# Kernel tuning notes

Measured on AMD Instinct MI355X. Metric: run time of the kernel, lower is better.

Reference implementation:

```python
import jax, jax.numpy as jnp
import numpy as np

B, L, HID, H, D = 1, 2048, 3072, 24, 128
MLP = 4 * HID
LH, LW = 32, 56      # latent mask grid -> LH*LW image tokens at the END of the sequence
LIP = 16             # IP-adapter image tokens
IP_SCALE = 0.6


def setup_inputs() -> dict:
    key = jax.random.key(0)
    k = jax.random.split(key, 10)
    # Flux rotary pe layout [1,1,L,D//2,2,2]: pe[...,0]=[cos,-sin], pe[...,1]=[sin,cos]
    pos = jnp.arange(L, dtype=jnp.float32)
    freqs = 1.0 / (10000.0 ** (jnp.arange(0, D, 2, dtype=jnp.float32) / D))
    ang = pos[:, None] * freqs[None, :]            # [L, D//2]
    cos, sin = jnp.cos(ang), jnp.sin(ang)
    pe = jnp.stack([jnp.stack([cos, -sin], -1), jnp.stack([sin, cos], -1)], -2)[None, None]
    return {
        "x": jax.random.normal(k[0], (B, L, HID), jnp.float32),
        "vec": jax.random.normal(k[1], (B, HID), jnp.float32),
        "pe": pe,
        "img_mask": jax.random.uniform(k[2], (B, LH, LW), jnp.float32),
        "image_emb": jax.random.normal(k[3], (B, LIP, HID), jnp.float32),
        "mod_w": jax.random.normal(k[4], (3 * HID, HID), jnp.float32) * 0.02,
        "mod_b": jnp.zeros((3 * HID,), jnp.float32),
        "lin1_w": jax.random.normal(k[5], (3 * HID + MLP, HID), jnp.float32) * 0.02,
        "lin1_b": jnp.zeros((3 * HID + MLP,), jnp.float32),
        "q_scale": jnp.ones((D,), jnp.float32),
        "k_scale": jnp.ones((D,), jnp.float32),
        "lin2_w": jax.random.normal(k[6], (HID, HID + MLP), jnp.float32) * 0.02,
        "lin2_b": jnp.zeros((HID,), jnp.float32),
        "ipk_w": jax.random.normal(k[7], (HID, HID), jnp.float32) * 0.02,
        "ipv_w": jax.random.normal(k[8], (HID, HID), jnp.float32) * 0.02,
    }


def _rms(x, scale, eps):
    # RMSNorm over last dim (QKNorm / norm_added_k)
    return x * jax.lax.rsqrt(jnp.mean(x * x, -1, keepdims=True) + eps) * scale


def _apply_rope(x, pe):
    # x: [B,H,L,D]; pe: [1,1,L,D//2,2,2]
    xr = x.reshape(x.shape[:-1] + (D // 2, 1, 2))
    out = pe[..., 0] * xr[..., 0] + pe[..., 1] * xr[..., 1]  # [B,H,L,D//2,2]
    return out.reshape(x.shape)


def _sdpa(q, k, v):
    # q:[B,H,Lq,D] k,v:[B,H,Lk,D] -> [B,Lq,H*D]
    s = jnp.einsum('bhqd,bhkd->bhqk', q, k) / jnp.sqrt(jnp.float32(D))
    o = jnp.einsum('bhqk,bhkd->bhqd', jax.nn.softmax(s, -1), v)
    return o.transpose(0, 2, 1, 3).reshape(q.shape[0], q.shape[2], H * D)


def reference(x, vec, pe, img_mask, image_emb, mod_w, mod_b, lin1_w, lin1_b,
              q_scale, k_scale, lin2_w, lin2_b, ipk_w, ipv_w):
    # modulation: SiLU(vec) -> Linear -> (shift, scale, gate), each [B,1,HID]
    mod = jax.nn.silu(vec) @ mod_w.T + mod_b
    shift, scale, gate = [m[:, None, :] for m in jnp.split(mod, 3, -1)]
    # pre_norm: LayerNorm, no affine, eps 1e-6 (biased variance, matches torch)
    ln = (x - jnp.mean(x, -1, keepdims=True)) * jax.lax.rsqrt(jnp.var(x, -1, keepdims=True) + 1e-6)
    x_mod = (1.0 + scale) * ln + shift
    # fused qkv + mlp projection
    h = x_mod @ lin1_w.T + lin1_b
    qkv, mlp = h[..., :3 * HID], h[..., 3 * HID:]
    q, k, v = qkv.reshape(B, L, 3, H, D).transpose(2, 0, 3, 1, 4)  # each [B,H,L,D]
    q = _rms(q, q_scale, 1e-6)
    k = _rms(k, k_scale, 1e-6)
    # rp_attention: RoPE then SDPA
    attn = _sdpa(_apply_rope(q, pe), _apply_rope(k, pe), v)       # [B,L,HID]
    # IP-adapter cross-attention: pre-rope q attends to projected image_emb
    ip_k = _rms((image_emb @ ipk_w.T).reshape(B, LIP, H, D).transpose(0, 2, 1, 3), 1.0, 1e-5)
    ip_v = (image_emb @ ipv_w.T).reshape(B, LIP, H, D).transpose(0, 2, 1, 3)
    ip_h = IP_SCALE * _sdpa(q, ip_k, ip_v)                        # [B,L,HID]
    # spatial mask applied to last LH*LW tokens, zeros elsewhere
    full_mask = jnp.concatenate(
        [jnp.zeros((B, L - LH * LW), ip_h.dtype), img_mask.reshape(B, LH * LW)], 1)
    attn = attn + ip_h * full_mask[..., None]
    out = jnp.concatenate([attn, jax.nn.gelu(mlp, approximate=True)], -1) @ lin2_w.T + lin2_b
    return x + gate * out
```

## Files before the change

kernel.cpp:

```cpp
#include <hip/hip_runtime.h>

#define HID 3072
#define LSEQ 2048
#define NH 24
#define HD 128
#define N1 21504
#define K2 15360

typedef unsigned short ushort_t;
typedef __attribute__((ext_vector_type(8))) short bf16x8;
typedef __attribute__((ext_vector_type(4))) float f32x4;

__device__ __forceinline__ unsigned short f2bf(float f) {
    union { float f; unsigned int u; } v; v.f = f;
    unsigned int u = v.u;
    u += 0x7fffu + ((u >> 16) & 1u);
    return (unsigned short)(u >> 16);
}
__device__ __forceinline__ float bf2f(unsigned short s) {
    union { unsigned int u; float f; } v; v.u = ((unsigned int)s) << 16;
    return v.f;
}
__device__ __forceinline__ float gelu_tanh(float x) {
    float u = 0.7978845608028654f * (x + 0.044715f * x * x * x);
    float t = 2.0f / (1.0f + __expf(-2.0f * u)) - 1.0f;
    return 0.5f * x * (1.0f + t);
}
__device__ __forceinline__ void gload_lds16(const ushort_t* g, ushort_t* l) {
    __builtin_amdgcn_global_load_lds((const __attribute__((address_space(1))) void*)g,
                                     (__attribute__((address_space(3))) void*)l, 16, 0, 0);
}

__global__ __launch_bounds__(256) void k_cvt(const float* __restrict__ src,
    ushort_t* __restrict__ dst, int n)
{
    int stride = gridDim.x * 256 * 8;
    for (int i = (blockIdx.x * 256 + threadIdx.x) * 8; i < n; i += stride) {
        float4 a = *reinterpret_cast<const float4*>(src + i);
        float4 b = *reinterpret_cast<const float4*>(src + i + 4);
        uint4 pk;
        pk.x = (unsigned)f2bf(a.x) | ((unsigned)f2bf(a.y) << 16);
        pk.y = (unsigned)f2bf(a.z) | ((unsigned)f2bf(a.w) << 16);
        pk.z = (unsigned)f2bf(b.x) | ((unsigned)f2bf(b.y) << 16);
        pk.w = (unsigned)f2bf(b.z) | ((unsigned)f2bf(b.w) << 16);
        *reinterpret_cast<uint4*>(dst + i) = pk;
    }
}

__global__ __launch_bounds__(256) void k_mod(const float* __restrict__ vec,
    const float* __restrict__ mw, const float* __restrict__ mb, float* __restrict__ mod) {
    __shared__ __align__(16) float sv[HID];
    int tid = threadIdx.x;
    for (int i = tid; i < HID; i += 256) {
        float v = vec[i];
        sv[i] = v / (1.0f + __expf(-v));
    }
    __syncthreads();
    int wave = tid >> 6, lane = tid & 63;
    int n = blockIdx.x * 4 + wave;
    const float* w = mw + (size_t)n * HID;
    float acc = 0.0f;
    for (int k = lane * 4; k < HID; k += 256) {
        float4 wv = *reinterpret_cast<const float4*>(w + k);
        float4 s  = *reinterpret_cast<const float4*>(sv + k);
        acc += wv.x * s.x + wv.y * s.y + wv.z * s.z + wv.w * s.w;
    }
    #pragma unroll
    for (int off = 1; off < 64; off <<= 1) acc += __shfl_xor(acc, off);
    if (lane == 0) mod[n] = acc + mb[n];
}

__global__ __launch_bounds__(256) void k_lnmod(const float* __restrict__ x,
    const float* __restrict__ mod, ushort_t* __restrict__ xmod) {
    int row = blockIdx.x, tid = threadIdx.x;
    const float4* xr = reinterpret_cast<const float4*>(x + (size_t)row * HID);
    float4 v[3];
    float s = 0.f, sq = 0.f;
    #pragma unroll
    for (int i = 0; i < 3; ++i) {
        v[i] = xr[tid + i * 256];
        s  += v[i].x + v[i].y + v[i].z + v[i].w;
        sq += v[i].x * v[i].x + v[i].y * v[i].y + v[i].z * v[i].z + v[i].w * v[i].w;
    }
    #pragma unroll
    for (int off = 1; off < 64; off <<= 1) { s += __shfl_xor(s, off); sq += __shfl_xor(sq, off); }
    __shared__ float rs[4], rq[4];
    int wave = tid >> 6, lane = tid & 63;
    if (lane == 0) { rs[wave] = s; rq[wave] = sq; }
    __syncthreads();
    s  = rs[0] + rs[1] + rs[2] + rs[3];
    sq = rq[0] + rq[1] + rq[2] + rq[3];
    float mean = s * (1.0f / HID);
    float var = sq * (1.0f / HID) - mean * mean;
    float rstd = rsqrtf(var + 1e-6f);
    ushort_t* orow = xmod + (size_t)row * HID;
    #pragma unroll
    for (int i = 0; i < 3; ++i) {
        int c = (tid + i * 256) * 4;
        float4 sc = *reinterpret_cast<const float4*>(mod + HID + c);
        float4 sh = *reinterpret_cast<const float4*>(mod + c);
        float o0 = (1.f + sc.x) * ((v[i].x - mean) * rstd) + sh.x;
        float o1 = (1.f + sc.y) * ((v[i].y - mean) * rstd) + sh.y;
        float o2 = (1.f + sc.z) * ((v[i].z - mean) * rstd) + sh.z;
        float o3 = (1.f + sc.w) * ((v[i].w - mean) * rstd) + sh.w;
        *reinterpret_cast<ushort4*>(orow + c) = make_ushort4(f2bf(o0), f2bf(o1), f2bf(o2), f2bf(o3));
    }
}

#define MFMA_CLUSTER(PH, AF)                                                          \
    do {                                                                              \
        __builtin_amdgcn_s_setprio(1);                                                \
        _Pragma("unroll") for (int i_ = 0; i_ < 2; ++i_)                              \
        _Pragma("unroll") for (int nj_ = 0; nj_ < 4; ++nj_)                           \
        _Pragma("unroll") for (int kh_ = 0; kh_ < 2; ++kh_)                           \
            acc[2 * (PH) + i_][nj_] = __builtin_amdgcn_mfma_f32_16x16x32_bf16(        \
                AF[i_][kh_], bfrag[nj_][kh_], acc[2 * (PH) + i_][nj_], 0, 0, 0);      \
        __builtin_amdgcn_s_setprio(0);                                                \
    } while (0)

template<int EPI>
__global__ __launch_bounds__(512) void k_gemm8(
    const ushort_t* __restrict__ A, const ushort_t* __restrict__ W,
    const float* __restrict__ bias, int Ks, int klen,
    ushort_t* __restrict__ out_qkv, ushort_t* __restrict__ out_concat,
    float* __restrict__ part)
{
    extern __shared__ __align__(16) char smem_raw[];
    ushort_t* smem = (ushort_t*)smem_raw;
    int tid = threadIdx.x;
    int wid = tid >> 6, l = tid & 63;
    int wm = wid >> 2, wn = wid & 3;
    int lr = l & 15, lg = l >> 4;

    int NTILE = (EPI == 1) ? 84 : 12;
    int flat = blockIdx.y * NTILE + blockIdx.x;
    int nf = (flat & 7) * NTILE + (flat >> 3);
    int mt = nf & 7, nt = nf >> 3;
    int m0 = mt * 256, n0 = nt * 256;
    int koff = blockIdx.z * klen;
    int NT = klen >> 6;

    int lrow = l >> 3;
    int lc   = (l & 7) ^ lrow;
    int arow_st = wm * 128 + wn * 32 + lrow;
    int bhalf = wn >> 1, ridx = wm * 2 + (wn & 1);
    int brow_st = bhalf * 128 + ridx * 32 + lrow;
    const ushort_t* aSrc = A + (size_t)(m0 + arow_st) * Ks + koff + lc * 8;
    const ushort_t* bSrc = W + (size_t)(n0 + brow_st) * Ks + koff + lc * 8;
    int aDst = (wm * 128 + wn * 32) * 64;
    int bDst = (bhalf * 128 + ridx * 32) * 64;

    auto stageA = [&](int t, int buf, int c) {
        gload_lds16(aSrc + (size_t)c * 8 * Ks + (size_t)t * 64,
                    smem + buf * 16384 + aDst + c * 512);
    };
    auto stageB = [&](int t, int c) {
        gload_lds16(bSrc + (size_t)c * 8 * Ks + (size_t)t * 64,
                    smem + 49152 + (t & 1) * 16384 + bDst + c * 512);
    };
    auto readA = [&](int buf, int row, int ccc) {
        return *reinterpret_cast<const bf16x8*>(smem + buf * 16384 + row * 64 + ((ccc ^ (row & 7)) << 3));
    };
    auto readB = [&](int p, int row, int ccc) {
        return *reinterpret_cast<const bf16x8*>(smem + 49152 + p * 16384 + row * 64 + ((ccc ^ (row & 7)) << 3));
    };

    f32x4 acc[8][4] = {};

    #pragma unroll
    for (int c = 0; c < 4; ++c) stageA(0, 0, c);
    #pragma unroll
    for (int c = 0; c < 4; ++c) stageB(0, c);
    #pragma unroll
    for (int c = 0; c < 4; ++c) stageA(1, 1, c);
    #pragma unroll
    for (int c = 0; c < 4; ++c) stageB(1, c);
    asm volatile("s_waitcnt vmcnt(8)" ::: "memory");
    __builtin_amdgcn_s_barrier();

    int pA = 0;
    int pA2 = 2;
    for (int t = 0; t < NT; ++t) {
        int pB = t & 1;
        bf16x8 bfrag[4][2], af0[2][2], af1[2][2], af2[2][2], af3[2][2];
        #pragma unroll
        for (int nj = 0; nj < 4; ++nj)
            #pragma unroll
            for (int kh = 0; kh < 2; ++kh)
                bfrag[nj][kh] = readB(pB, wn * 64 + nj * 16 + lr, kh * 4 + lg);
        #pragma unroll
        for (int i = 0; i < 2; ++i)
            #pragma unroll
            for (int kh = 0; kh < 2; ++kh)
                af0[i][kh] = readA(pA, wm * 128 + i * 16 + lr, kh * 4 + lg);
        if (t + 2 < NT) {
            stageA(t + 2, pA2, 0); stageA(t + 2, pA2, 1);
            stageA(t + 2, pA2, 2); stageA(t + 2, pA2, 3);
        }
        #pragma unroll
        for (int i = 0; i < 2; ++i)
            #pragma unroll
            for (int kh = 0; kh < 2; ++kh)
                af1[i][kh] = readA(pA, wm * 128 + (2 + i) * 16 + lr, kh * 4 + lg);
        MFMA_CLUSTER(0, af0);
        #pragma unroll
        for (int i = 0; i < 2; ++i)
            #pragma unroll
            for (int kh = 0; kh < 2; ++kh)
                af2[i][kh] = readA(pA, wm * 128 + (4 + i) * 16 + lr, kh * 4 + lg);
        MFMA_CLUSTER(1, af1);
        __builtin_amdgcn_s_barrier();
        if (t + 2 < NT) {
            stageB(t + 2, 0); stageB(t + 2, 1);
            stageB(t + 2, 2); stageB(t + 2, 3);
        }
        #pragma unroll
        for (int i = 0; i < 2; ++i)
            #pragma unroll
            for (int kh = 0; kh < 2; ++kh)
                af3[i][kh] = readA(pA, wm * 128 + (6 + i) * 16 + lr, kh * 4 + lg);
        MFMA_CLUSTER(2, af2);
        MFMA_CLUSTER(3, af3);
        if (t + 2 < NT)      asm volatile("s_waitcnt vmcnt(8)" ::: "memory");
        else if (t + 1 < NT) asm volatile("s_waitcnt vmcnt(0)" ::: "memory");
        __builtin_amdgcn_s_barrier();
        pA  = (pA  + 1 == 3) ? 0 : pA  + 1;
        pA2 = (pA2 + 1 == 3) ? 0 : pA2 + 1;
    }

    #pragma unroll
    for (int nj = 0; nj < 4; ++nj) {
        int col = n0 + wn * 64 + nj * 16 + lr;
        float b = (EPI == 1) ? bias[col] : 0.f;
        #pragma unroll
        for (int mi = 0; mi < 8; ++mi) {
            int rbase = m0 + wm * 128 + mi * 16 + lg * 4;
            #pragma unroll
            for (int r = 0; r < 4; ++r) {
                int mrow = rbase + r;
                float val = acc[mi][nj][r] + b;
                if (EPI == 1) {
                    if (col < 3 * HID) {
                        out_qkv[(size_t)mrow * (3 * HID) + col] = f2bf(val);
                    } else {
                        out_concat[(size_t)mrow * K2 + HID + (col - 3 * HID)] = f2bf(gelu_tanh(val));
                    }
                } else {
                    part[(size_t)blockIdx.z * LSEQ * HID + (size_t)mrow * HID + col] = val;
                }
            }
        }
    }
}

__global__ __launch_bounds__(256) void k_red(const float* __restrict__ part,
    const float* __restrict__ bias, const float* __restrict__ xres,
    const float* __restrict__ mod, float* __restrict__ dout)
{
    size_t base = ((size_t)blockIdx.x * 256 + threadIdx.x) * 4;
    int col = (int)(base % HID);
    float4 s = *reinterpret_cast<const float4*>(part + base);
    #pragma unroll
    for (int z = 1; z < 8; ++z) {
        float4 p = *reinterpret_cast<const float4*>(part + (size_t)z * LSEQ * HID + base);
        s.x += p.x; s.y += p.y; s.z += p.z; s.w += p.w;
    }
    float4 bb = *reinterpret_cast<const float4*>(bias + col);
    float4 gg = *reinterpret_cast<const float4*>(mod + 2 * HID + col);
    float4 xx = *reinterpret_cast<const float4*>(xres + base);
    float4 o;
    o.x = xx.x + gg.x * (s.x + bb.x);
    o.y = xx.y + gg.y * (s.y + bb.y);
    o.z = xx.z + gg.z * (s.z + bb.z);
    o.w = xx.w + gg.w * (s.w + bb.w);
    *reinterpret_cast<float4*>(dout + base) = o;
}

__global__ __launch_bounds__(256) void k_qkv(const ushort_t* __restrict__ qkv,
    const float* __restrict__ pe, const float* __restrict__ q_scale, const float* __restrict__ k_scale,
    ushort_t* __restrict__ q_rope, ushort_t* __restrict__ k_rope,
    ushort_t* __restrict__ q_rms, ushort_t* __restrict__ v_t)
{
    __shared__ ushort_t vtile[64][132];
    int h = blockIdx.y, l0 = blockIdx.x * 64;
    int wave = threadIdx.x >> 6, lane = threadIdx.x & 63;
    int d0 = lane * 2;
    float qs0 = q_scale[d0], qs1 = q_scale[d0 + 1];
    float ks0 = k_scale[d0], ks1 = k_scale[d0 + 1];
    for (int it = 0; it < 16; ++it) {
        int ll = it * 4 + wave;
        int l = l0 + ll;
        const ushort_t* base = qkv + (size_t)l * (3 * HID) + h * HD + d0;
        unsigned qw = *reinterpret_cast<const unsigned*>(base);
        unsigned kw = *reinterpret_cast<const unsigned*>(base + HID);
        unsigned vw = *reinterpret_cast<const unsigned*>(base + 2 * HID);
        float qx = bf2f((ushort_t)(qw & 0xffffu)), qy = bf2f((ushort_t)(qw >> 16));
        float kx = bf2f((ushort_t)(kw & 0xffffu)), ky = bf2f((ushort_t)(kw >> 16));
        float sq = qx * qx + qy * qy;
        float sk = kx * kx + ky * ky;
        #pragma unroll
        for (int off = 1; off < 64; off <<= 1) { sq += __shfl_xor(sq, off); sk += __shfl_xor(sk, off); }
        float rqv = rsqrtf(sq * (1.0f / HD) + 1e-6f);
        float rkv = rsqrtf(sk * (1.0f / HD) + 1e-6f);
        float qnx = qx * rqv * qs0, qny = qy * rqv * qs1;
        float knx = kx * rkv * ks0, kny = ky * rkv * ks1;
        float4 p = *reinterpret_cast<const float4*>(pe + ((size_t)l * 64 + lane) * 4);
        size_t off_hl = ((size_t)h * LSEQ + l) * HD + d0;
        *reinterpret_cast<unsigned*>(q_rms + off_hl) = (unsigned)f2bf(qnx) | ((unsigned)f2bf(qny) << 16);
        float qrx = p.x * qnx + p.y * qny, qry = p.z * qnx + p.w * qny;
        float krx = p.x * knx + p.y * kny, kry = p.z * knx + p.w * kny;
        *reinterpret_cast<unsigned*>(q_rope + off_hl) = (unsigned)f2bf(qrx) | ((unsigned)f2bf(qry) << 16);
        *reinterpret_cast<unsigned*>(k_rope + off_hl) = (unsigned)f2bf(krx) | ((unsigned)f2bf(kry) << 16);
        vtile[ll][d0] = (ushort_t)(vw & 0xffffu);
        vtile[ll][d0 + 1] = (ushort_t)(vw >> 16);
    }
    __syncthreads();
    int d = threadIdx.x >> 1, half = threadIdx.x & 1;
    ushort_t* dst = v_t + ((size_t)h * HD + d) * LSEQ + l0 + half * 32;
    #pragma unroll
    for (int g = 0; g < 4; ++g) {
        unsigned w0, w1, w2, w3;
        int lb = half * 32 + g * 8;
        w0 = (unsigned)vtile[lb + 0][d] | ((unsigned)vtile[lb + 1][d] << 16);
        w1 = (unsigned)vtile[lb + 2][d] | ((unsigned)vtile[lb + 3][d] << 16);
        w2 = (unsigned)vtile[lb + 4][d] | ((unsigned)vtile[lb + 5][d] << 16);
        w3 = (unsigned)vtile[lb + 6][d] | ((unsigned)vtile[lb + 7][d] << 16);
        reinterpret_cast<uint4*>(dst)[g] = make_uint4(w0, w1, w2, w3);
    }
}

__global__ __launch_bounds__(256) void k_ipgemv(const float* __restrict__ emb,
    const float* __restrict__ wk, const float* __restrict__ wv,
    float* __restrict__ ipk, float* __restrict__ ipv)
{
    int task = blockIdx.x * 4 + (threadIdx.x >> 6);
    int lane = threadIdx.x & 63;
    int which = task / HID;
    int n = task % HID;
    const float* w = (which ? wv : wk) + (size_t)n * HID;
    float acc[16];
    #pragma unroll
    for (int t = 0; t < 16; ++t) acc[t] = 0.f;
    for (int k = lane; k < HID; k += 64) {
        float wval = w[k];
        #pragma unroll
        for (int t = 0; t < 16; ++t) acc[t] += emb[t * HID + k] * wval;
    }
    #pragma unroll
    for (int off = 1; off < 64; off <<= 1) {
        #pragma unroll
        for (int t = 0; t < 16; ++t) acc[t] += __shfl_xor(acc[t], off);
    }
    if (lane == 0) {
        int hh = n >> 7, d = n & 127;
        float* dstp = which ? ipv : ipk;
        #pragma unroll
        for (int t = 0; t < 16; ++t) dstp[((size_t)hh * 16 + t) * HD + d] = acc[t];
    }
}

__global__ __launch_bounds__(256) void k_ipkrms(float* __restrict__ ipk) {
    int row = blockIdx.x * 4 + (threadIdx.x >> 6);
    int lane = threadIdx.x & 63;
    float2 v = *reinterpret_cast<const float2*>(ipk + (size_t)row * HD + lane * 2);
    float sq = v.x * v.x + v.y * v.y;
    #pragma unroll
    for (int off = 1; off < 64; off <<= 1) sq += __shfl_xor(sq, off);
    float r = rsqrtf(sq * (1.0f / HD) + 1e-5f);
    float2 o; o.x = v.x * r; o.y = v.y * r;
    *reinterpret_cast<float2*>(ipk + (size_t)row * HD + lane * 2) = o;
}

__global__ __launch_bounds__(256) void k_attn(const ushort_t* __restrict__ q_rope,
    const ushort_t* __restrict__ k_rope, const ushort_t* __restrict__ v_t,
    float* __restrict__ attnbuf)
{
    __shared__ __align__(16) ushort_t Ks[32 * 128];
    __shared__ __align__(16) ushort_t Vs[128 * 32];
    __shared__ __align__(16) ushort_t Ps[4 * 32 * 40];
    const float SC = 0.08838834764831845f;
    int h = blockIdx.y, q0 = blockIdx.x * 128;
    int tid = threadIdx.x, wave = tid >> 6, lane = tid & 63;
    int lr = lane & 15, lg = lane >> 4;
    const ushort_t* Kb = k_rope + (size_t)h * LSEQ * HD;
    const ushort_t* Vb = v_t + (size_t)h * HD * LSEQ;
    bf16x8 qf[2][4];
    #pragma unroll
    for (int i = 0; i < 2; ++i) {
        #pragma unroll
        for (int ks = 0; ks < 4; ++ks) {
            int row = q0 + wave * 32 + i * 16 + lr;
            int d = ks * 32 + lg * 8;
            qf[i][ks] = *reinterpret_cast<const bf16x8*>(q_rope + ((size_t)h * LSEQ + row) * HD + d);
        }
    }
    f32x4 o[2][8] = {};
    float mrun[2][4], lrun[2][4];
    #pragma unroll
    for (int i = 0; i < 2; ++i)
        #pragma unroll
        for (int r = 0; r < 4; ++r) { mrun[i][r] = -1e30f; lrun[i][r] = 0.f; }

    for (int kt = 0; kt < LSEQ; kt += 32) {
        #pragma unroll
        for (int ii = 0; ii < 2; ++ii) {
            int c = tid + ii * 256;
            int krow = c >> 4, kc = c & 15;
            uint4 va = *reinterpret_cast<const uint4*>(Kb + (size_t)(kt + krow) * HD + kc * 8);
            *reinterpret_cast<uint4*>(reinterpret_cast<char*>(Ks) + krow * 256 + ((kc ^ (krow & 15)) << 4)) = va;
            int dr = c >> 2, vc = c & 3;
            uint4 vb = *reinterpret_cast<const uint4*>(Vb + (size_t)dr * LSEQ + kt + vc * 8);
            *reinterpret_cast<uint4*>(reinterpret_cast<char*>(Vs) + dr * 64 + ((vc ^ ((dr >> 1) & 3)) << 4)) = vb;
        }
        __syncthreads();
        f32x4 s[2][2] = {};
        #pragma unroll
        for (int ks = 0; ks < 4; ++ks) {
            bf16x8 kf[2];
            #pragma unroll
            for (int j = 0; j < 2; ++j) {
                int krow = j * 16 + lr;
                int cc = ks * 4 + lg;
                kf[j] = *reinterpret_cast<const bf16x8*>(reinterpret_cast<char*>(Ks) + krow * 256 + ((cc ^ (krow & 15)) << 4));
            }
            #pragma unroll
            for (int i = 0; i < 2; ++i)
                #pragma unroll
                for (int j = 0; j < 2; ++j)
                    s[i][j] = __builtin_amdgcn_mfma_f32_16x16x32_bf16(qf[i][ks], kf[j], s[i][j], 0, 0, 0);
        }
        float alpha[2][4];
        #pragma unroll
        for (int i = 0; i < 2; ++i) {
            #pragma unroll
            for (int r = 0; r < 4; ++r) {
                float v0 = s[i][0][r] * SC, v1 = s[i][1][r] * SC;
                float mx = fmaxf(v0, v1);
                #pragma unroll
                for (int off = 1; off < 16; off <<= 1) mx = fmaxf(mx, __shfl_xor(mx, off));
                float mnew = fmaxf(mrun[i][r], mx);
                float al = __expf(mrun[i][r] - mnew);
                float p0 = __expf(v0 - mnew), p1 = __expf(v1 - mnew);
                float rs2 = p0 + p1;
                #pragma unroll
                for (int off = 1; off < 16; off <<= 1) rs2 += __shfl_xor(rs2, off);
                lrun[i][r] = lrun[i][r] * al + rs2;
                mrun[i][r] = mnew;
                alpha[i][r] = al;
                s[i][0][r] = p0; s[i][1][r] = p1;
            }
        }
        #pragma unroll
        for (int i = 0; i < 2; ++i)
            #pragma unroll
            for (int j8 = 0; j8 < 8; ++j8)
                #pragma unroll
                for (int r = 0; r < 4; ++r) o[i][j8][r] *= alpha[i][r];
        #pragma unroll
        for (int i = 0; i < 2; ++i)
            #pragma unroll
            for (int j = 0; j < 2; ++j)
                #pragma unroll
                for (int r = 0; r < 4; ++r) {
                    int ql = i * 16 + lg * 4 + r;
                    int kp = j * 16 + lr;
                    Ps[wave * 1280 + ql * 40 + kp] = f2bf(s[i][j][r]);
                }
        __syncthreads();
        bf16x8 pa[2];
        #pragma unroll
        for (int i = 0; i < 2; ++i)
            pa[i] = *reinterpret_cast<const bf16x8*>(Ps + wave * 1280 + (i * 16 + lr) * 40 + lg * 8);
        #pragma unroll
        for (int j8 = 0; j8 < 8; ++j8) {
            int d = j8 * 16 + lr;
            bf16x8 vf = *reinterpret_cast<const bf16x8*>(reinterpret_cast<char*>(Vs) + d * 64 + ((lg ^ ((d >> 1) & 3)) << 4));
            #pragma unroll
            for (int i = 0; i < 2; ++i)
                o[i][j8] = __builtin_amdgcn_mfma_f32_16x16x32_bf16(pa[i], vf, o[i][j8], 0, 0, 0);
        }
        __syncthreads();
    }
    #pragma unroll
    for (int i = 0; i < 2; ++i) {
        #pragma unroll
        for (int r = 0; r < 4; ++r) {
            float inv = 1.0f / lrun[i][r];
            int mrow = q0 + wave * 32 + i * 16 + lg * 4 + r;
            float* orow = attnbuf + (size_t)mrow * HID + h * HD;
            #pragma unroll
            for (int j8 = 0; j8 < 8; ++j8)
                orow[j8 * 16 + lr] = o[i][j8][r] * inv;
        }
    }
}

__global__ __launch_bounds__(256) void k_ipattn(const ushort_t* __restrict__ q_rms,
    const float* __restrict__ ipk, const float* __restrict__ ipv,
    const float* __restrict__ attnbuf, const float* __restrict__ img_mask,
    ushort_t* __restrict__ concat)
{
    int task = blockIdx.x * 4 + (threadIdx.x >> 6);
    int lane = threadIdx.x & 63;
    int h = task >> 11;
    int l = task & 2047;
    int d0 = lane * 2;
    float2 a = *reinterpret_cast<const float2*>(attnbuf + (size_t)l * HID + h * HD + d0);
    if (l >= 256) {
        float mask = img_mask[l - 256];
        unsigned qv = *reinterpret_cast<const unsigned*>(q_rms + ((size_t)h * LSEQ + l) * HD + d0);
        float qx = bf2f((unsigned short)(qv & 0xffffu)), qy = bf2f((unsigned short)(qv >> 16));
        float s[16];
        const float* kb = ipk + (size_t)h * 16 * HD + d0;
        #pragma unroll
        for (int j = 0; j < 16; ++j) {
            float2 kk = *reinterpret_cast<const float2*>(kb + j * HD);
            float part = qx * kk.x + qy * kk.y;
            #pragma unroll
            for (int off = 1; off < 64; off <<= 1) part += __shfl_xor(part, off);
            s[j] = part * 0.08838834764831845f;
        }
        float mx = s[0];
        #pragma unroll
        for (int j = 1; j < 16; ++j) mx = fmaxf(mx, s[j]);
        float sum = 0.f;
        #pragma unroll
        for (int j = 0; j < 16; ++j) { s[j] = __expf(s[j] - mx); sum += s[j]; }
        float ox = 0.f, oy = 0.f;
        const float* vb = ipv + (size_t)h * 16 * HD + d0;
        #pragma unroll
        for (int j = 0; j < 16; ++j) {
            float2 vv = *reinterpret_cast<const float2*>(vb + j * HD);
            ox += s[j] * vv.x; oy += s[j] * vv.y;
        }
        float f = 0.6f * mask / sum;
        a.x += f * ox; a.y += f * oy;
    }
    *reinterpret_cast<unsigned*>(concat + (size_t)l * K2 + h * HD + d0) =
        (unsigned)f2bf(a.x) | ((unsigned)f2bf(a.y) << 16);
}

extern "C" void kernel_launch(void* const* d_in, const int* in_sizes, int n_in,
                              void* d_out, int out_size, void* d_ws, size_t ws_size,
                              hipStream_t stream)
{
    (void)in_sizes; (void)n_in; (void)out_size; (void)ws_size;
    const float* x         = (const float*)d_in[0];
    const float* vec       = (const float*)d_in[1];
    const float* pe        = (const float*)d_in[2];
    const float* img_mask  = (const float*)d_in[3];
    const float* image_emb = (const float*)d_in[4];
    const float* mod_w     = (const float*)d_in[5];
    const float* mod_b     = (const float*)d_in[6];
    const float* lin1_w    = (const float*)d_in[7];
    const float* lin1_b    = (const float*)d_in[8];
    const float* q_scale   = (const float*)d_in[9];
    const float* k_scale   = (const float*)d_in[10];
    const float* lin2_w    = (const float*)d_in[11];
    const float* lin2_b    = (const float*)d_in[12];
    const float* ipk_w     = (const float*)d_in[13];
    const float* ipv_w     = (const float*)d_in[14];
    float* dout = (float*)d_out;

    char* wp = (char*)d_ws;
    auto alloc = [&](size_t bytes) { char* p = wp; wp += (bytes + 255) & ~(size_t)255; return p; };
    float*    mod     = (float*)   alloc((size_t)9216 * 4);
    ushort_t* concat  = (ushort_t*)alloc((size_t)LSEQ * K2 * 2);
    ushort_t* lin2_bf = (ushort_t*)alloc((size_t)HID * K2 * 2);
    float*    ipk     = (float*)   alloc((size_t)NH * 16 * HD * 4);
    float*    ipv     = (float*)   alloc((size_t)NH * 16 * HD * 4);
    char* ubase = wp;
    ushort_t* lin1_bf = (ushort_t*)alloc((size_t)N1 * HID * 2);
    ushort_t* xmod    = (ushort_t*)alloc((size_t)LSEQ * HID * 2);
    ushort_t* qkv     = (ushort_t*)alloc((size_t)LSEQ * 3 * HID * 2);
    float*    attnbuf = (float*)   alloc((size_t)LSEQ * HID * 4);
    ushort_t* q_rope  = (ushort_t*)alloc((size_t)NH * LSEQ * HD * 2);
    ushort_t* k_rope  = (ushort_t*)alloc((size_t)NH * LSEQ * HD * 2);
    ushort_t* q_rms   = (ushort_t*)alloc((size_t)NH * LSEQ * HD * 2);
    ushort_t* v_t     = (ushort_t*)alloc((size_t)NH * HD * LSEQ * 2);
    float*    partial = (float*)ubase;

    hipFuncSetAttribute((const void*)k_gemm8<1>, hipFuncAttributeMaxDynamicSharedMemorySize, 163840);
    hipFuncSetAttribute((const void*)k_gemm8<0>, hipFuncAttributeMaxDynamicSharedMemorySize, 163840);

    k_cvt   <<<dim3(2048), dim3(256), 0, stream>>>(lin1_w, lin1_bf, N1 * HID);
    k_cvt   <<<dim3(2048), dim3(256), 0, stream>>>(lin2_w, lin2_bf, HID * K2);
    k_mod   <<<dim3(9216 / 4), dim3(256), 0, stream>>>(vec, mod_w, mod_b, mod);
    k_lnmod <<<dim3(LSEQ), dim3(256), 0, stream>>>(x, mod, xmod);
    k_gemm8<1><<<dim3(84, 8, 1), dim3(512), 163840, stream>>>(xmod, lin1_bf, lin1_b, HID, HID,
                                                              qkv, concat, nullptr);
    k_qkv   <<<dim3(32, NH), dim3(256), 0, stream>>>(qkv, pe, q_scale, k_scale,
                                                     q_rope, k_rope, q_rms, v_t);
    k_ipgemv<<<dim3(2 * HID / 4), dim3(256), 0, stream>>>(image_emb, ipk_w, ipv_w, ipk, ipv);
    k_ipkrms<<<dim3(NH * 16 / 4), dim3(256), 0, stream>>>(ipk);
    k_attn  <<<dim3(16, NH), dim3(256), 0, stream>>>(q_rope, k_rope, v_t, attnbuf);
    k_ipattn<<<dim3(NH * LSEQ / 4), dim3(256), 0, stream>>>(q_rms, ipk, ipv, attnbuf, img_mask, concat);
    k_gemm8<0><<<dim3(12, 8, 8), dim3(512), 163840, stream>>>(concat, lin2_bf, nullptr, K2, 1920,
                                                              nullptr, nullptr, partial);
    k_red   <<<dim3(LSEQ * HID / 1024), dim3(256), 0, stream>>>(partial, lin2_b, x, mod, dout);
}
```

Measured before the change: 1.160 ms.

## Restructure GEMM pipeline: double-buffer A, triple-buffer B, prefetch B fragments per K-half

Changes the GEMM main loop's buffering so A uses two LDS buffers and is prefetched one tile ahead, while B uses three buffers and is prefetched two tiles ahead. B fragments are now split by K-half, and the first half for the next tile is read from LDS before the current tile finishes. MFMA clusters are reordered to run all kh=0 products before kh=1. The aim is to overlap LDS reads of B with MFMA work and cut live fragment registers. The trade-off is a shallower prefetch distance for A, which can expose global-load latency.

```diff
diff --git a/kernel.cpp b/kernel.cpp
--- a/kernel.cpp
+++ b/kernel.cpp
@@ -107,14 +107,17 @@
     }
 }
 
-#define MFMA_CLUSTER(PH, AF)                                                          \
+#define MFMA_KH(PH, AF)                                                               \
     do {                                                                              \
         __builtin_amdgcn_s_setprio(1);                                                \
         _Pragma("unroll") for (int i_ = 0; i_ < 2; ++i_)                              \
         _Pragma("unroll") for (int nj_ = 0; nj_ < 4; ++nj_)                           \
-        _Pragma("unroll") for (int kh_ = 0; kh_ < 2; ++kh_)                           \
             acc[2 * (PH) + i_][nj_] = __builtin_amdgcn_mfma_f32_16x16x32_bf16(        \
-                AF[i_][kh_], bfrag[nj_][kh_], acc[2 * (PH) + i_][nj_], 0, 0, 0);      \
+                AF[i_][0], bk0[nj_], acc[2 * (PH) + i_][nj_], 0, 0, 0);               \
+        _Pragma("unroll") for (int i_ = 0; i_ < 2; ++i_)                              \
+        _Pragma("unroll") for (int nj_ = 0; nj_ < 4; ++nj_)                           \
+            acc[2 * (PH) + i_][nj_] = __builtin_amdgcn_mfma_f32_16x16x32_bf16(        \
+                AF[i_][1], bk1[nj_], acc[2 * (PH) + i_][nj_], 0, 0, 0);               \
         __builtin_amdgcn_s_setprio(0);                                                \
     } while (0)
 
@@ -150,82 +153,88 @@
     int aDst = (wm * 128 + wn * 32) * 64;
     int bDst = (bhalf * 128 + ridx * 32) * 64;
 
-    auto stageA = [&](int t, int buf, int c) {
-        gload_lds16(aSrc + (size_t)c * 8 * Ks + (size_t)t * 64,
-                    smem + buf * 16384 + aDst + c * 512);
+    auto stageA = [&](int t) {
+        #pragma unroll
+        for (int c = 0; c < 4; ++c)
+            gload_lds16(aSrc + (size_t)c * 8 * Ks + (size_t)t * 64,
+                        smem + (t & 1) * 16384 + aDst + c * 512);
     };
-    auto stageB = [&](int t, int c) {
-        gload_lds16(bSrc + (size_t)c * 8 * Ks + (size_t)t * 64,
-                    smem + 49152 + (t & 1) * 16384 + bDst + c * 512);
+    auto stageB = [&](int t, int buf) {
+        #pragma unroll
+        for (int c = 0; c < 4; ++c)
+            gload_lds16(bSrc + (size_t)c * 8 * Ks + (size_t)t * 64,
+                        smem + 32768 + buf * 16384 + bDst + c * 512);
     };
-    auto readA = [&](int buf, int row, int ccc) {
-        return *reinterpret_cast<const bf16x8*>(smem + buf * 16384 + row * 64 + ((ccc ^ (row & 7)) << 3));
+    auto readA = [&](int p, int row, int ccc) {
+        return *reinterpret_cast<const bf16x8*>(smem + p * 16384 + row * 64 + ((ccc ^ (row & 7)) << 3));
     };
-    auto readB = [&](int p, int row, int ccc) {
-        return *reinterpret_cast<const bf16x8*>(smem + 49152 + p * 16384 + row * 64 + ((ccc ^ (row & 7)) << 3));
+    auto readB = [&](int q, int row, int ccc) {
+        return *reinterpret_cast<const bf16x8*>(smem + 32768 + q * 16384 + row * 64 + ((ccc ^ (row & 7)) << 3));
     };
 
     f32x4 acc[8][4] = {};
-
-    #pragma unroll
-    for (int c = 0; c < 4; ++c) stageA(0, 0, c);
-    #pragma unroll
-    for (int c = 0; c < 4; ++c) stageB(0, c);
-    #pragma unroll
-    for (int c = 0; c < 4; ++c) stageA(1, 1, c);
-    #pragma unroll
-    for (int c = 0; c < 4; ++c) stageB(1, c);
-    asm volatile("s_waitcnt vmcnt(8)" ::: "memory");
+    bf16x8 bk0[4], bk1[4], bk0n[4];
+
+    stageA(0);
+    stageB(0, 0);
+    stageB(1, 1);
+    asm volatile("s_waitcnt vmcnt(4)" ::: "memory");
     __builtin_amdgcn_s_barrier();
-
-    int pA = 0;
-    int pA2 = 2;
+    #pragma unroll
+    for (int nj = 0; nj < 4; ++nj)
+        bk0[nj] = readB(0, wn * 64 + nj * 16 + lr, lg);
+
+    int pB0 = 0, pB1 = 1, pB2 = 2;
     for (int t = 0; t < NT; ++t) {
-        int pB = t & 1;
-        bf16x8 bfrag[4][2], af0[2][2], af1[2][2], af2[2][2], af3[2][2];
+        int pA = t & 1;
         #pragma unroll
         for (int nj = 0; nj < 4; ++nj)
-            #pragma unroll
-            for (int kh = 0; kh < 2; ++kh)
-                bfrag[nj][kh] = readB(pB, wn * 64 + nj * 16 + lr, kh * 4 + lg);
+            bk1[nj] = readB(pB0, wn * 64 + nj * 16 + lr, 4 + lg);
+        bf16x8 af0[2][2];
         #pragma unroll
         for (int i = 0; i < 2; ++i)
             #pragma unroll
             for (int kh = 0; kh < 2; ++kh)
                 af0[i][kh] = readA(pA, wm * 128 + i * 16 + lr, kh * 4 + lg);
-        if (t + 2 < NT) {
-            stageA(t + 2, pA2, 0); stageA(t + 2, pA2, 1);
-            stageA(t + 2, pA2, 2); stageA(t + 2, pA2, 3);
-        }
+        if (t + 1 < NT) stageA(t + 1);
+        MFMA_KH(0, af0);
+        bf16x8 af1[2][2];
         #pragma unroll
         for (int i = 0; i < 2; ++i)
             #pragma unroll
             for (int kh = 0; kh < 2; ++kh)
                 af1[i][kh] = readA(pA, wm * 128 + (2 + i) * 16 + lr, kh * 4 + lg);
-        MFMA_CLUSTER(0, af0);
+        MFMA_KH(1, af1);
+        if (t + 1 < NT) asm volatile("s_waitcnt vmcnt(4)" ::: "memory");
+        __builtin_amdgcn_s_barrier();
+        if (t + 1 < NT) {
+            #pragma unroll
+            for (int nj = 0; nj < 4; ++nj)
+                bk0n[nj] = readB(pB1, wn * 64 + nj * 16 + lr, lg);
+        }
+        if (t + 2 < NT) stageB(t + 2, pB2);
+        bf16x8 af2[2][2];
         #pragma unroll
         for (int i = 0; i < 2; ++i)
             #pragma unroll
             for (int kh = 0; kh < 2; ++kh)
                 af2[i][kh] = readA(pA, wm * 128 + (4 + i) * 16 + lr, kh * 4 + lg);
-        MFMA_CLUSTER(1, af1);
-        __builtin_amdgcn_s_barrier();
-        if (t + 2 < NT) {
-            stageB(t + 2, 0); stageB(t + 2, 1);
-            stageB(t + 2, 2); stageB(t + 2, 3);
-        }
+        MFMA_KH(2, af2);
+        bf16x8 af3[2][2];
         #pragma unroll
         for (int i = 0; i < 2; ++i)
             #pragma unroll
             for (int kh = 0; kh < 2; ++kh)
                 af3[i][kh] = readA(pA, wm * 128 + (6 + i) * 16 + lr, kh * 4 + lg);
-        MFMA_CLUSTER(2, af2);
-        MFMA_CLUSTER(3, af3);
-        if (t + 2 < NT)      asm volatile("s_waitcnt vmcnt(8)" ::: "memory");
-        else if (t + 1 < NT) asm volatile("s_waitcnt vmcnt(0)" ::: "memory");
+        MFMA_KH(3, af3);
+        if (t + 1 < NT) {
+            if (t + 2 < NT) asm volatile("s_waitcnt vmcnt(4)" ::: "memory");
+            else            asm volatile("s_waitcnt vmcnt(0)" ::: "memory");
+        }
         __builtin_amdgcn_s_barrier();
-        pA  = (pA  + 1 == 3) ? 0 : pA  + 1;
-        pA2 = (pA2 + 1 == 3) ? 0 : pA2 + 1;
+        #pragma unroll
+        for (int nj = 0; nj < 4; ++nj) bk0[nj] = bk0n[nj];
+        int tmp = pB0; pB0 = pB1; pB1 = pB2; pB2 = tmp;
     }
 
     #pragma unroll
```

Result: no change. 1.169 ms (median of 2 runs) (+0.8%).
